# Kernel tuning notes

Hardware: AMD Instinct MI355X
Metric: run time of the kernel (lower is better)

Reference implementation:

```python
import jax, jax.numpy as jnp
import numpy as np

SEQ_LEN = 8192
SIGMA = 2.0
COUNT_WEIGHT = 0.1
PEAK_PROB = 0.002  # ~16 peaks per sequence
LOG_CLAMP = -100.0  # torch F.binary_cross_entropy clamps log to -100


def setup_inputs() -> dict:
    key = jax.random.key(0)
    k1, k2 = jax.random.split(key)
    B = 32
    pred = jax.random.uniform(k1, (B, SEQ_LEN, 1), dtype=jnp.float32,
                              minval=1e-6, maxval=1.0 - 1e-6)
    # sparse binary peak indicator, as in radar pulse labels
    target = (jax.random.uniform(k2, (B, SEQ_LEN, 1)) < PEAK_PROB).astype(jnp.float32)
    return {"pred": pred, "target": target}


def _gaussian_target(target):
    # target: [B, T, 1]; original loops over every (b, t) peak and adds a
    # full-length gaussian centered at t. Vectorized: mask[B,T] @ K[T,T].
    T = target.shape[1]
    t_idx = jnp.arange(T, dtype=jnp.float32)
    K = jnp.exp(-0.5 * ((t_idx[None, :] - t_idx[:, None]) / SIGMA) ** 2)  # [T, T]
    mask = (target[:, :, 0] > 0).astype(jnp.float32)                      # [B, T]
    g = jnp.einsum("bt,ts->bs", mask, K)                                  # [B, T]
    return jnp.clip(g, 0.0, 1.0)[:, :, None]                              # [B, T, 1]


def reference(pred, target):
    gt = _gaussian_target(target)
    # binary_cross_entropy (mean reduction) with torch-style log clamping
    log_p = jnp.maximum(jnp.log(pred), LOG_CLAMP)
    log_1mp = jnp.maximum(jnp.log1p(-pred), LOG_CLAMP)
    bce_loss = -jnp.mean(gt * log_p + (1.0 - gt) * log_1mp)

    pred_peaks = (pred > 0.5).astype(jnp.float32)
    count_diff = jnp.abs(pred_peaks.sum(axis=1) - target.sum(axis=1))  # [B, 1]
    count_loss = COUNT_WEIGHT * jnp.mean(count_diff)

    total_loss = bce_loss + count_loss
    return total_loss, bce_loss, count_loss
```

## Files before the change

kernel.cpp:

```cpp
#include <hip/hip_runtime.h>


#define BATCH    32
#define SEQ_T    8192
#define CHUNK    1024
#define NCHUNKS  (SEQ_T / CHUNK)
#define NBLOCKS  (BATCH * NCHUNKS)
#define HALO     32
#define KTAB     67
#define MAXPEAKS 64
#define NTHREADS 256

__global__ __launch_bounds__(NTHREADS) void pulse_loss_main(
    const float* __restrict__ pred,
    const float* __restrict__ tgt,
    float* __restrict__ ws)
{
    const int tid = threadIdx.x;
    const int blk = blockIdx.x;
    const int b   = blk >> 3;
    const int c0  = (blk & 7) * CHUNK;
    const float* __restrict__ prow = pred + (size_t)b * SEQ_T;
    const float* __restrict__ trow = tgt  + (size_t)b * SEQ_T;

    __shared__ int   s_npeaks;
    __shared__ int   s_peaks[MAXPEAKS];
    __shared__ float s_K[KTAB];
    __shared__ float s_bce[NTHREADS / 64];
    __shared__ int   s_cnt[NTHREADS / 64];

    if (tid == 0) s_npeaks = 0;
    if (tid < KTAB) {
        float d = (float)(tid - 33);
        s_K[tid] = __expf(-0.125f * d * d);
    }
    __syncthreads();

    int cnt_t = 0;
    for (int i = tid; i < CHUNK + 2 * HALO; i += NTHREADS) {
        int gi = c0 - HALO + i;
        if (gi >= 0 && gi < SEQ_T) {
            if (trow[gi] > 0.0f) {
                int idx = atomicAdd(&s_npeaks, 1);
                if (idx < MAXPEAKS) s_peaks[idx] = gi;
                if (gi >= c0 && gi < c0 + CHUNK) cnt_t++;
            }
        }
    }
    __syncthreads();
    const int np = min(s_npeaks, MAXPEAKS);

    const float4 p4 = ((const float4*)(prow + c0))[tid];
    float bce  = 0.0f;
    int   dcnt = -cnt_t;
    #pragma unroll
    for (int j = 0; j < 4; ++j) {
        const float p = (j == 0) ? p4.x : (j == 1) ? p4.y : (j == 2) ? p4.z : p4.w;
        const int   i = c0 + tid * 4 + j;
        float g = 0.0f;
        for (int k = 0; k < np; ++k) {
            int d = i - s_peaks[k];
            d = min(max(d, -33), 33);
            g += s_K[d + 33];
        }
        g = fminf(g, 1.0f);
        float lp  = fmaxf(__logf(p),        -100.0f);
        float l1p = fmaxf(__logf(1.0f - p), -100.0f);
        bce  += l1p + g * (lp - l1p);
        dcnt += (p > 0.5f) ? 1 : 0;
    }

    #pragma unroll
    for (int off = 32; off > 0; off >>= 1) {
        bce  += __shfl_down(bce,  off);
        dcnt += __shfl_down(dcnt, off);
    }
    const int wid  = tid >> 6;
    const int lane = tid & 63;
    if (lane == 0) { s_bce[wid] = bce; s_cnt[wid] = dcnt; }
    __syncthreads();

    if (tid == 0) {
        float tb = 0.0f;
        int   tc = 0;
        #pragma unroll
        for (int w = 0; w < NTHREADS / 64; ++w) { tb += s_bce[w]; tc += s_cnt[w]; }
        ws[blk] = tb;
        ((int*)ws)[NBLOCKS + blk] = tc;
    }
}

__global__ __launch_bounds__(NBLOCKS) void pulse_loss_finalize(
    const float* __restrict__ ws,
    float* __restrict__ out)
{
    const int t = threadIdx.x;
    float bce = ws[t];
    int   dc  = ((const int*)ws)[NBLOCKS + t];

    dc += __shfl_down(dc, 4, 8);
    dc += __shfl_down(dc, 2, 8);
    dc += __shfl_down(dc, 1, 8);
    float ad = ((t & 7) == 0) ? fabsf((float)dc) : 0.0f;

    #pragma unroll
    for (int off = 32; off > 0; off >>= 1) {
        bce += __shfl_down(bce, off);
        ad  += __shfl_down(ad,  off);
    }

    __shared__ float s_b[4], s_a[4];
    const int wid  = t >> 6;
    const int lane = t & 63;
    if (lane == 0) { s_b[wid] = bce; s_a[wid] = ad; }
    __syncthreads();

    if (t == 0) {
        float sb = 0.0f, sd = 0.0f;
        #pragma unroll
        for (int w = 0; w < 4; ++w) { sb += s_b[w]; sd += s_a[w]; }
        float bce_loss   = -sb / (float)(BATCH * SEQ_T);
        float count_loss = 0.1f * sd / (float)BATCH;
        out[0] = bce_loss + count_loss;
        out[1] = bce_loss;
        out[2] = count_loss;
    }
}

extern "C" void kernel_launch(void* const* d_in, const int* in_sizes, int n_in,
                              void* d_out, int out_size, void* d_ws, size_t ws_size,
                              hipStream_t stream) {
    const float* pred = (const float*)d_in[0];
    const float* tgt  = (const float*)d_in[1];
    float*       out  = (float*)d_out;
    float*       ws   = (float*)d_ws;

    pulse_loss_main<<<dim3(NBLOCKS), dim3(NTHREADS), 0, stream>>>(pred, tgt, ws);
    pulse_loss_finalize<<<dim3(1), dim3(NBLOCKS), 0, stream>>>(ws, out);
}
```

Baseline: 11.61 us.

## Fuse finalize into main kernel using per-block flags and spin-wait block

Replaces the two-kernel launch with a single kernel. Block 0 spin-waits on per-block release flags in the workspace, then does the final reduction, while the other blocks publish partial sums with atomic stores. This removes the second launch and the gap between kernels. It relies on the worker blocks being scheduled while block 0 spins; that holds here because the grid has only 257 blocks. It also relies on the workspace flags starting cleared, since they are reset only after being read and nothing zeroes them before the first call.

```diff
diff --git a/kernel.cpp b/kernel.cpp
--- a/kernel.cpp
+++ b/kernel.cpp
@@ -4,20 +4,70 @@
 #define BATCH    32
 #define SEQ_T    8192
 #define CHUNK    1024
-#define NCHUNKS  (SEQ_T / CHUNK)
-#define NBLOCKS  (BATCH * NCHUNKS)
+#define NWORK    (BATCH * (SEQ_T / CHUNK))
 #define HALO     32
 #define KTAB     67
 #define MAXPEAKS 64
 #define NTHREADS 256
+#define FLAG_MAGIC 0x5CA1AB1E
 
-__global__ __launch_bounds__(NTHREADS) void pulse_loss_main(
+
+__global__ __launch_bounds__(NTHREADS) void pulse_loss_one(
     const float* __restrict__ pred,
     const float* __restrict__ tgt,
+    float* __restrict__ out,
     float* __restrict__ ws)
 {
     const int tid = threadIdx.x;
-    const int blk = blockIdx.x;
+    float* ws_f = ws;
+    int*   ws_i = (int*)ws;
+
+    if (blockIdx.x == 0) {
+        int* flags = ws_i + 2 * NWORK;
+        const int t = tid;
+
+        while (__hip_atomic_load(&flags[t], __ATOMIC_ACQUIRE,
+                                 __HIP_MEMORY_SCOPE_AGENT) != FLAG_MAGIC) {
+            __builtin_amdgcn_s_sleep(2);
+        }
+        float bce = __hip_atomic_load(&ws_f[t], __ATOMIC_RELAXED,
+                                      __HIP_MEMORY_SCOPE_AGENT);
+        int   dc  = __hip_atomic_load(&ws_i[NWORK + t], __ATOMIC_RELAXED,
+                                      __HIP_MEMORY_SCOPE_AGENT);
+        __hip_atomic_store(&flags[t], 0, __ATOMIC_RELAXED,
+                           __HIP_MEMORY_SCOPE_AGENT);
+
+        dc += __shfl_down(dc, 4, 8);
+        dc += __shfl_down(dc, 2, 8);
+        dc += __shfl_down(dc, 1, 8);
+        float ad = ((t & 7) == 0) ? fabsf((float)dc) : 0.0f;
+
+        #pragma unroll
+        for (int off = 32; off > 0; off >>= 1) {
+            bce += __shfl_down(bce, off);
+            ad  += __shfl_down(ad,  off);
+        }
+
+        __shared__ float s_b[4], s_a[4];
+        const int wid  = t >> 6;
+        const int lane = t & 63;
+        if (lane == 0) { s_b[wid] = bce; s_a[wid] = ad; }
+        __syncthreads();
+
+        if (t == 0) {
+            float sb = 0.0f, sd = 0.0f;
+            #pragma unroll
+            for (int w = 0; w < 4; ++w) { sb += s_b[w]; sd += s_a[w]; }
+            float bce_loss   = -sb / (float)(BATCH * SEQ_T);
+            float count_loss = 0.1f * sd / (float)BATCH;
+            out[0] = bce_loss + count_loss;
+            out[1] = bce_loss;
+            out[2] = count_loss;
+        }
+        return;
+    }
+
+    const int blk = blockIdx.x - 1;
     const int b   = blk >> 3;
     const int c0  = (blk & 7) * CHUNK;
     const float* __restrict__ prow = pred + (size_t)b * SEQ_T;
@@ -85,45 +135,12 @@
         int   tc = 0;
         #pragma unroll
         for (int w = 0; w < NTHREADS / 64; ++w) { tb += s_bce[w]; tc += s_cnt[w]; }
-        ws[blk] = tb;
-        ((int*)ws)[NBLOCKS + blk] = tc;
-    }
-}
-
-__global__ __launch_bounds__(NBLOCKS) void pulse_loss_finalize(
-    const float* __restrict__ ws,
-    float* __restrict__ out)
-{
-    const int t = threadIdx.x;
-    float bce = ws[t];
-    int   dc  = ((const int*)ws)[NBLOCKS + t];
-
-    dc += __shfl_down(dc, 4, 8);
-    dc += __shfl_down(dc, 2, 8);
-    dc += __shfl_down(dc, 1, 8);
-    float ad = ((t & 7) == 0) ? fabsf((float)dc) : 0.0f;
-
-    #pragma unroll
-    for (int off = 32; off > 0; off >>= 1) {
-        bce += __shfl_down(bce, off);
-        ad  += __shfl_down(ad,  off);
-    }
-
-    __shared__ float s_b[4], s_a[4];
-    const int wid  = t >> 6;
-    const int lane = t & 63;
-    if (lane == 0) { s_b[wid] = bce; s_a[wid] = ad; }
-    __syncthreads();
-
-    if (t == 0) {
-        float sb = 0.0f, sd = 0.0f;
-        #pragma unroll
-        for (int w = 0; w < 4; ++w) { sb += s_b[w]; sd += s_a[w]; }
-        float bce_loss   = -sb / (float)(BATCH * SEQ_T);
-        float count_loss = 0.1f * sd / (float)BATCH;
-        out[0] = bce_loss + count_loss;
-        out[1] = bce_loss;
-        out[2] = count_loss;
+        __hip_atomic_store(&ws_f[blk], tb, __ATOMIC_RELAXED,
+                           __HIP_MEMORY_SCOPE_AGENT);
+        __hip_atomic_store(&ws_i[NWORK + blk], tc, __ATOMIC_RELAXED,
+                           __HIP_MEMORY_SCOPE_AGENT);
+        __hip_atomic_store(&ws_i[2 * NWORK + blk], FLAG_MAGIC, __ATOMIC_RELEASE,
+                           __HIP_MEMORY_SCOPE_AGENT);
     }
 }
 
@@ -135,6 +152,6 @@
     float*       out  = (float*)d_out;
     float*       ws   = (float*)d_ws;
 
-    pulse_loss_main<<<dim3(NBLOCKS), dim3(NTHREADS), 0, stream>>>(pred, tgt, ws);
-    pulse_loss_finalize<<<dim3(1), dim3(NBLOCKS), 0, stream>>>(ws, out);
+    pulse_loss_one<<<dim3(NWORK + 1), dim3(NTHREADS), 0, stream>>>(
+        pred, tgt, out, ws);
 }
```

After: 11.86 us. 2.2% more time.
